# Kernel optimization log

Hardware: AMD Instinct MI355X
Metric: run time of the kernel (lower is better)

## Reference

```python
import jax, jax.numpy as jnp
import numpy as np

EPS = 1e-5


def setup_inputs() -> dict:
    key = jax.random.key(0)
    ks = jax.random.split(key, 8)
    b, n, l, e = 2, 16, 1024, 512
    qd, kd, vd = 64, 64, 64
    x = jax.random.normal(ks[0], (b, n, l, e), dtype=jnp.float32)
    past_kv = jax.random.normal(ks[1], (b, n, kd, vd), dtype=jnp.float32)
    s = 1.0 / np.sqrt(e)
    Wq = jax.random.normal(ks[2], (qd, e), dtype=jnp.float32) * s
    bq = jnp.zeros((qd,), dtype=jnp.float32)
    Wk = jax.random.normal(ks[3], (kd, e), dtype=jnp.float32) * s
    bk = jnp.zeros((kd,), dtype=jnp.float32)
    Wv = jax.random.normal(ks[4], (vd, e), dtype=jnp.float32) * s
    bv = jnp.zeros((vd,), dtype=jnp.float32)
    return {"x": x, "past_kv": past_kv, "Wq": Wq, "bq": bq,
            "Wk": Wk, "bk": bk, "Wv": Wv, "bv": bv}


def reference(x, past_kv, Wq, bq, Wk, bk, Wv, bv):
    b, n, l, e = x.shape
    # QKV projections on the last axis: [b,n,l,e] -> [b,n,l,d]
    q = jnp.einsum('bnle,de->bnld', x, Wq) + bq
    k = jnp.einsum('bnle,de->bnld', x, Wk) + bk
    v = jnp.einsum('bnle,de->bnld', x, Wv) + bv
    # RetNet per-head decay: 1 - 2^(-5-h), shape [1,n,1,1,1]
    decay = 1.0 - jnp.exp2(-5.0 - jnp.arange(n, dtype=jnp.float32))
    decay = decay.reshape(1, n, 1, 1, 1)
    # decayed state + per-position outer product k_t (x) v_t -> [b,n,l,kd,vd]
    current_kv = decay * past_kv[:, :, None, :, :] + k[..., :, None] * v[..., None, :]
    # Q-weighted reduction over k_dim -> [b,n,l,vd]
    out = jnp.einsum('bnlk,bnlkv->bnlv', q, current_kv)
    # F.group_norm(out, num_groups=n): per (b, head), normalize over (l, vd)
    mean = jnp.mean(out, axis=(2, 3), keepdims=True)
    var = jnp.var(out, axis=(2, 3), keepdims=True)
    out = (out - mean) * jax.lax.rsqrt(var + EPS)
    return out, current_kv
```

## Files before the change

### kernel.cpp

```cpp
#include <hip/hip_runtime.h>


constexpr int B  = 2;
constexpr int NH = 16;
constexpr int L  = 1024;
constexpr int E  = 512;
constexpr int D  = 64;
constexpr int M  = B * NH * L;
constexpr int NQKV = 192;
constexpr int BLK = 16;
constexpr int NBLKS = M / BLK;
constexpr float EPS = 1e-5f;

using short8 = __attribute__((ext_vector_type(8))) short;
using f32x4  = __attribute__((ext_vector_type(4))) float;

__device__ __forceinline__ unsigned short f2bf(float f) {
    union { float f; unsigned int u; } x; x.f = f;
    unsigned int u = x.u;
    return (unsigned short)((u + 0x7fffu + ((u >> 16) & 1u)) >> 16);
}

__global__ __launch_bounds__(256) void convw_kernel(
    const float* __restrict__ Wq, const float* __restrict__ Wk,
    const float* __restrict__ Wv, unsigned short* __restrict__ Wb)
{
    int idx = blockIdx.x * 256 + threadIdx.x;
    const float* src = (idx < 8192) ? Wq : (idx < 16384) ? Wk : Wv;
    int off = idx & 8191;
    float4 v = ((const float4*)src)[off];
    unsigned short o[4] = {f2bf(v.x), f2bf(v.y), f2bf(v.z), f2bf(v.w)};
    Wb[(size_t)idx * 4 + 0] = o[0];
    Wb[(size_t)idx * 4 + 1] = o[1];
    Wb[(size_t)idx * 4 + 2] = o[2];
    Wb[(size_t)idx * 4 + 3] = o[3];
}

__global__ __launch_bounds__(512) void proj_mfma_kernel(
    const float* __restrict__ x, const unsigned short* __restrict__ Wb,
    const float* __restrict__ bq, const float* __restrict__ bk,
    const float* __restrict__ bv,
    float* __restrict__ qkv)
{
    constexpr int BM = 128, BK = 64, LDP = 72;
    __shared__ unsigned short Xs[BM][LDP];
    __shared__ unsigned short Ws[NQKV][LDP];
    __shared__ float bias_s[NQKV];

    const int tid  = threadIdx.x;
    const int row0 = blockIdx.x * BM;
    if (tid < NQKV)
        bias_s[tid] = (tid < 64) ? bq[tid] : (tid < 128) ? bk[tid - 64] : bv[tid - 128];

    const int wid  = tid >> 6;
    const int lane = tid & 63;
    const int wr   = wid >> 2;
    const int wc   = wid & 3;
    const int l15  = lane & 15;
    const int lk   = (lane >> 4) * 8;

    const int xr = tid >> 2;
    const int xc = (tid & 3) * 16;

    f32x4 acc[4][3] = {};

    for (int k0 = 0; k0 < E; k0 += BK) {
        float4 xa[4];
        #pragma unroll
        for (int i = 0; i < 4; ++i)
            xa[i] = *(const float4*)&x[(size_t)(row0 + xr) * E + k0 + xc + i * 4];
        short8 wch[3];
        #pragma unroll
        for (int i = 0; i < 3; ++i) {
            int c = tid + i * 512;
            wch[i] = *(const short8*)&Wb[(size_t)(c >> 3) * E + k0 + (c & 7) * 8];
        }
        __syncthreads();
        unsigned short tmp[16];
        #pragma unroll
        for (int i = 0; i < 4; ++i) {
            tmp[i*4+0] = f2bf(xa[i].x); tmp[i*4+1] = f2bf(xa[i].y);
            tmp[i*4+2] = f2bf(xa[i].z); tmp[i*4+3] = f2bf(xa[i].w);
        }
        *(short8*)&Xs[xr][xc]     = *(short8*)&tmp[0];
        *(short8*)&Xs[xr][xc + 8] = *(short8*)&tmp[8];
        #pragma unroll
        for (int i = 0; i < 3; ++i) {
            int c = tid + i * 512;
            *(short8*)&Ws[c >> 3][(c & 7) * 8] = wch[i];
        }
        __syncthreads();

        #pragma unroll
        for (int kk = 0; kk < 2; ++kk) {
            short8 a[4], b[3];
            #pragma unroll
            for (int mi = 0; mi < 4; ++mi)
                a[mi] = *(const short8*)&Xs[wr * 64 + mi * 16 + l15][kk * 32 + lk];
            #pragma unroll
            for (int ni = 0; ni < 3; ++ni)
                b[ni] = *(const short8*)&Ws[wc * 48 + ni * 16 + l15][kk * 32 + lk];
            #pragma unroll
            for (int mi = 0; mi < 4; ++mi)
                #pragma unroll
                for (int ni = 0; ni < 3; ++ni)
                    acc[mi][ni] = __builtin_amdgcn_mfma_f32_16x16x32_bf16(
                        a[mi], b[ni], acc[mi][ni], 0, 0, 0);
        }
    }

    #pragma unroll
    for (int mi = 0; mi < 4; ++mi) {
        #pragma unroll
        for (int ni = 0; ni < 3; ++ni) {
            int col = wc * 48 + ni * 16 + l15;
            float bb = bias_s[col];
            #pragma unroll
            for (int j = 0; j < 4; ++j) {
                int row = wr * 64 + mi * 16 + (lane >> 4) * 4 + j;
                qkv[(size_t)(row0 + row) * NQKV + col] = acc[mi][ni][j] + bb;
            }
        }
    }
}

__global__ __launch_bounds__(256) void retention_kernel(
    const float* __restrict__ qkv,
    const float* __restrict__ past_kv,
    float* __restrict__ out_pre,
    float* __restrict__ ckv,
    float* __restrict__ partials)
{
    const int blk  = blockIdx.x;
    const int bn   = blk >> 6;
    const int pos0 = (blk & 63) * BLK;
    const int h    = bn & (NH - 1);
    const int tid  = threadIdx.x;
    const float decay = 1.0f - exp2f(-5.0f - (float)h);

    __shared__ float pkv_s[64 * 64];
    __shared__ float qkv_s[BLK * NQKV];
    __shared__ float qk_s[BLK];
    __shared__ float r1[256], r2[256];

    const float* pkv = past_kv + (size_t)bn * 4096;
    #pragma unroll
    for (int j = 0; j < 4; ++j) {
        int f = tid + j * 256;
        *(float4*)&pkv_s[f * 4] = *(const float4*)&pkv[f * 4];
    }
    const float* qrow = qkv + (size_t)(bn * L + pos0) * NQKV;
    #pragma unroll
    for (int j = 0; j < 3; ++j) {
        int f = tid + j * 256;
        *(float4*)&qkv_s[f * 4] = *(const float4*)&qrow[f * 4];
    }
    __syncthreads();

    {
        int pos = tid >> 4, c = tid & 15;
        const float* qp = &qkv_s[pos * NQKV];
        float p = 0.0f;
        #pragma unroll
        for (int j = 0; j < 4; ++j)
            p = fmaf(qp[c * 4 + j], qp[64 + c * 4 + j], p);
        p += __shfl_xor(p, 1); p += __shfl_xor(p, 2);
        p += __shfl_xor(p, 4); p += __shfl_xor(p, 8);
        if (c == 0) qk_s[pos] = p;
    }

    float4 p4[4];
    #pragma unroll
    for (int j = 0; j < 4; ++j)
        p4[j] = *(const float4*)&pkv_s[(tid + j * 256) * 4];
    __syncthreads();

    float* co = ckv + (size_t)(bn * L + pos0) * 4096;
    for (int pos = 0; pos < BLK; ++pos) {
        const float* ks = &qkv_s[pos * NQKV + 64];
        const float* vs = &qkv_s[pos * NQKV + 128];
        #pragma unroll
        for (int j = 0; j < 4; ++j) {
            int f = tid + j * 256;
            float kk = ks[f >> 4];
            float4 vv = *(const float4*)&vs[(f & 15) * 4];
            float4 r;
            r.x = fmaf(decay, p4[j].x, kk * vv.x);
            r.y = fmaf(decay, p4[j].y, kk * vv.y);
            r.z = fmaf(decay, p4[j].z, kk * vv.z);
            r.w = fmaf(decay, p4[j].w, kk * vv.w);
            *(float4*)&co[(size_t)pos * 4096 + f * 4] = r;
        }
    }

    const int wave = tid >> 6, vd = tid & 63;
    float accs[4] = {0.0f, 0.0f, 0.0f, 0.0f};
    for (int kd = 0; kd < 64; ++kd) {
        float pv = pkv_s[kd * 64 + vd];
        #pragma unroll
        for (int pp = 0; pp < 4; ++pp)
            accs[pp] = fmaf(qkv_s[(wave + pp * 4) * NQKV + kd], pv, accs[pp]);
    }
    float s1 = 0.0f, s2 = 0.0f;
    #pragma unroll
    for (int pp = 0; pp < 4; ++pp) {
        int pos = wave + pp * 4;
        float o = fmaf(decay, accs[pp],
                       qk_s[pos] * qkv_s[pos * NQKV + 128 + vd]);
        out_pre[(size_t)(bn * L + pos0 + pos) * D + vd] = o;
        s1 += o; s2 += o * o;
    }

    r1[tid] = s1; r2[tid] = s2;
    __syncthreads();
    for (int off = 128; off; off >>= 1) {
        if (tid < off) { r1[tid] += r1[tid + off]; r2[tid] += r2[tid + off]; }
        __syncthreads();
    }
    if (tid == 0) {
        partials[(size_t)blk * 2]     = r1[0];
        partials[(size_t)blk * 2 + 1] = r2[0];
    }
}

__global__ __launch_bounds__(64) void group_reduce_kernel(
    const float* __restrict__ partials, float* __restrict__ stats)
{
    const int g   = blockIdx.x;
    const int tid = threadIdx.x;
    float s1 = partials[(size_t)(g * 64 + tid) * 2];
    float s2 = partials[(size_t)(g * 64 + tid) * 2 + 1];
    #pragma unroll
    for (int off = 32; off; off >>= 1) {
        s1 += __shfl_down(s1, off);
        s2 += __shfl_down(s2, off);
    }
    if (tid == 0) {
        const float cnt = (float)(L * D);
        float mean = s1 / cnt;
        float var  = s2 / cnt - mean * mean;
        stats[g * 2]     = mean;
        stats[g * 2 + 1] = rsqrtf(var + EPS);
    }
}

__global__ __launch_bounds__(256) void normalize_kernel(
    float* __restrict__ out, const float* __restrict__ stats)
{
    int idx = blockIdx.x * 256 + threadIdx.x;
    int g = idx >> 14;
    float mean = stats[g * 2];
    float rstd = stats[g * 2 + 1];
    float4 v = ((const float4*)out)[idx];
    v.x = (v.x - mean) * rstd; v.y = (v.y - mean) * rstd;
    v.z = (v.z - mean) * rstd; v.w = (v.w - mean) * rstd;
    ((float4*)out)[idx] = v;
}

extern "C" void kernel_launch(void* const* d_in, const int* in_sizes, int n_in,
                              void* d_out, int out_size, void* d_ws, size_t ws_size,
                              hipStream_t stream)
{
    const float* x       = (const float*)d_in[0];
    const float* past_kv = (const float*)d_in[1];
    const float* Wq      = (const float*)d_in[2];
    const float* bq      = (const float*)d_in[3];
    const float* Wk      = (const float*)d_in[4];
    const float* bk      = (const float*)d_in[5];
    const float* Wv      = (const float*)d_in[6];
    const float* bv      = (const float*)d_in[7];

    float* out = (float*)d_out;
    float* ckv = out + (size_t)M * 64;

    unsigned short* Wb = (unsigned short*)(ckv + (size_t)M * 4096) - (size_t)NQKV * E;

    float* qkv      = (float*)d_ws;
    float* partials = qkv + (size_t)M * 192;
    float* stats    = partials + (size_t)NBLKS * 2;

    convw_kernel<<<96, 256, 0, stream>>>(Wq, Wk, Wv, Wb);
    proj_mfma_kernel<<<M / 128, 512, 0, stream>>>(x, Wb, bq, bk, bv, qkv);
    retention_kernel<<<NBLKS, 256, 0, stream>>>(qkv, past_kv, out, ckv, partials);
    group_reduce_kernel<<<32, 64, 0, stream>>>(partials, stats);
    normalize_kernel<<<(M * 16) / 256, 256, 0, stream>>>(out, stats);
}
```

Before: 146.8 us.

## Fuse QKV projection MFMA into retention kernel, drop qkv workspace round trip

```diff
diff --git a/kernel.cpp b/kernel.cpp
--- a/kernel.cpp
+++ b/kernel.cpp
@@ -29,108 +29,29 @@
     const float* src = (idx < 8192) ? Wq : (idx < 16384) ? Wk : Wv;
     int off = idx & 8191;
     float4 v = ((const float4*)src)[off];
-    unsigned short o[4] = {f2bf(v.x), f2bf(v.y), f2bf(v.z), f2bf(v.w)};
-    Wb[(size_t)idx * 4 + 0] = o[0];
-    Wb[(size_t)idx * 4 + 1] = o[1];
-    Wb[(size_t)idx * 4 + 2] = o[2];
-    Wb[(size_t)idx * 4 + 3] = o[3];
-}
-
-__global__ __launch_bounds__(512) void proj_mfma_kernel(
-    const float* __restrict__ x, const unsigned short* __restrict__ Wb,
+    Wb[(size_t)idx * 4 + 0] = f2bf(v.x);
+    Wb[(size_t)idx * 4 + 1] = f2bf(v.y);
+    Wb[(size_t)idx * 4 + 2] = f2bf(v.z);
+    Wb[(size_t)idx * 4 + 3] = f2bf(v.w);
+}
+
+__global__ __launch_bounds__(256) void fused_kernel(
+    const float* __restrict__ x,
+    const unsigned short* __restrict__ Wb,
     const float* __restrict__ bq, const float* __restrict__ bk,
     const float* __restrict__ bv,
-    float* __restrict__ qkv)
-{
-    constexpr int BM = 128, BK = 64, LDP = 72;
-    __shared__ unsigned short Xs[BM][LDP];
-    __shared__ unsigned short Ws[NQKV][LDP];
-    __shared__ float bias_s[NQKV];
-
-    const int tid  = threadIdx.x;
-    const int row0 = blockIdx.x * BM;
-    if (tid < NQKV)
-        bias_s[tid] = (tid < 64) ? bq[tid] : (tid < 128) ? bk[tid - 64] : bv[tid - 128];
-
-    const int wid  = tid >> 6;
-    const int lane = tid & 63;
-    const int wr   = wid >> 2;
-    const int wc   = wid & 3;
-    const int l15  = lane & 15;
-    const int lk   = (lane >> 4) * 8;
-
-    const int xr = tid >> 2;
-    const int xc = (tid & 3) * 16;
-
-    f32x4 acc[4][3] = {};
-
-    for (int k0 = 0; k0 < E; k0 += BK) {
-        float4 xa[4];
-        #pragma unroll
-        for (int i = 0; i < 4; ++i)
-            xa[i] = *(const float4*)&x[(size_t)(row0 + xr) * E + k0 + xc + i * 4];
-        short8 wch[3];
-        #pragma unroll
-        for (int i = 0; i < 3; ++i) {
-            int c = tid + i * 512;
-            wch[i] = *(const short8*)&Wb[(size_t)(c >> 3) * E + k0 + (c & 7) * 8];
-        }
-        __syncthreads();
-        unsigned short tmp[16];
-        #pragma unroll
-        for (int i = 0; i < 4; ++i) {
-            tmp[i*4+0] = f2bf(xa[i].x); tmp[i*4+1] = f2bf(xa[i].y);
-            tmp[i*4+2] = f2bf(xa[i].z); tmp[i*4+3] = f2bf(xa[i].w);
-        }
-        *(short8*)&Xs[xr][xc]     = *(short8*)&tmp[0];
-        *(short8*)&Xs[xr][xc + 8] = *(short8*)&tmp[8];
-        #pragma unroll
-        for (int i = 0; i < 3; ++i) {
-            int c = tid + i * 512;
-            *(short8*)&Ws[c >> 3][(c & 7) * 8] = wch[i];
-        }
-        __syncthreads();
-
-        #pragma unroll
-        for (int kk = 0; kk < 2; ++kk) {
-            short8 a[4], b[3];
-            #pragma unroll
-            for (int mi = 0; mi < 4; ++mi)
-                a[mi] = *(const short8*)&Xs[wr * 64 + mi * 16 + l15][kk * 32 + lk];
-            #pragma unroll
-            for (int ni = 0; ni < 3; ++ni)
-                b[ni] = *(const short8*)&Ws[wc * 48 + ni * 16 + l15][kk * 32 + lk];
-            #pragma unroll
-            for (int mi = 0; mi < 4; ++mi)
-                #pragma unroll
-                for (int ni = 0; ni < 3; ++ni)
-                    acc[mi][ni] = __builtin_amdgcn_mfma_f32_16x16x32_bf16(
-                        a[mi], b[ni], acc[mi][ni], 0, 0, 0);
-        }
-    }
-
-    #pragma unroll
-    for (int mi = 0; mi < 4; ++mi) {
-        #pragma unroll
-        for (int ni = 0; ni < 3; ++ni) {
-            int col = wc * 48 + ni * 16 + l15;
-            float bb = bias_s[col];
-            #pragma unroll
-            for (int j = 0; j < 4; ++j) {
-                int row = wr * 64 + mi * 16 + (lane >> 4) * 4 + j;
-                qkv[(size_t)(row0 + row) * NQKV + col] = acc[mi][ni][j] + bb;
-            }
-        }
-    }
-}
-
-__global__ __launch_bounds__(256) void retention_kernel(
-    const float* __restrict__ qkv,
     const float* __restrict__ past_kv,
     float* __restrict__ out_pre,
     float* __restrict__ ckv,
     float* __restrict__ partials)
 {
+    constexpr int LDP = 520;
+    __shared__ unsigned short Xs[BLK][LDP];
+    __shared__ float qkv_s[BLK * NQKV];
+    __shared__ float bias_s[NQKV];
+    __shared__ float qk_s[BLK];
+    __shared__ float r1[256], r2[256];
+
     const int blk  = blockIdx.x;
     const int bn   = blk >> 6;
     const int pos0 = (blk & 63) * BLK;
@@ -138,22 +59,53 @@
     const int tid  = threadIdx.x;
     const float decay = 1.0f - exp2f(-5.0f - (float)h);
 
-    __shared__ float pkv_s[64 * 64];
-    __shared__ float qkv_s[BLK * NQKV];
-    __shared__ float qk_s[BLK];
-    __shared__ float r1[256], r2[256];
+    if (tid < NQKV)
+        bias_s[tid] = (tid < 64) ? bq[tid] : (tid < 128) ? bk[tid - 64] : bv[tid - 128];
+
+    const float* xrow = x + (size_t)(bn * L + pos0) * E;
+    #pragma unroll
+    for (int j = 0; j < 8; ++j) {
+        int f   = tid + j * 256;
+        int row = f >> 7;
+        int c4  = f & 127;
+        float4 xv = *(const float4*)&xrow[f * 4];
+        unsigned short hlf[4] = {f2bf(xv.x), f2bf(xv.y), f2bf(xv.z), f2bf(xv.w)};
+        *(uint2*)&Xs[row][c4 * 4] = *(uint2*)hlf;
+    }
 
     const float* pkv = past_kv + (size_t)bn * 4096;
-    #pragma unroll
-    for (int j = 0; j < 4; ++j) {
-        int f = tid + j * 256;
-        *(float4*)&pkv_s[f * 4] = *(const float4*)&pkv[f * 4];
-    }
-    const float* qrow = qkv + (size_t)(bn * L + pos0) * NQKV;
-    #pragma unroll
-    for (int j = 0; j < 3; ++j) {
-        int f = tid + j * 256;
-        *(float4*)&qkv_s[f * 4] = *(const float4*)&qrow[f * 4];
+    float4 p4[4];
+    #pragma unroll
+    for (int j = 0; j < 4; ++j)
+        p4[j] = *(const float4*)&pkv[(tid + j * 256) * 4];
+
+    __syncthreads();
+
+    const int wid  = tid >> 6;
+    const int lane = tid & 63;
+    const int l15  = lane & 15;
+    const int lkE  = (lane >> 4) * 8;
+
+    f32x4 acc[3] = {};
+    #pragma unroll 4
+    for (int kt = 0; kt < 16; ++kt) {
+        short8 a = *(const short8*)&Xs[l15][kt * 32 + lkE];
+        #pragma unroll
+        for (int ni = 0; ni < 3; ++ni) {
+            int col = wid * 48 + ni * 16 + l15;
+            short8 b = *(const short8*)&Wb[(size_t)col * E + kt * 32 + lkE];
+            acc[ni] = __builtin_amdgcn_mfma_f32_16x16x32_bf16(a, b, acc[ni], 0, 0, 0);
+        }
+    }
+    #pragma unroll
+    for (int ni = 0; ni < 3; ++ni) {
+        int col = wid * 48 + ni * 16 + l15;
+        float bb = bias_s[col];
+        #pragma unroll
+        for (int j = 0; j < 4; ++j) {
+            int pos = (lane >> 4) * 4 + j;
+            qkv_s[pos * NQKV + col] = acc[ni][j] + bb;
+        }
     }
     __syncthreads();
 
@@ -168,11 +120,6 @@
         p += __shfl_xor(p, 4); p += __shfl_xor(p, 8);
         if (c == 0) qk_s[pos] = p;
     }
-
-    float4 p4[4];
-    #pragma unroll
-    for (int j = 0; j < 4; ++j)
-        p4[j] = *(const float4*)&pkv_s[(tid + j * 256) * 4];
     __syncthreads();
 
     float* co = ckv + (size_t)(bn * L + pos0) * 4096;
@@ -195,8 +142,9 @@
 
     const int wave = tid >> 6, vd = tid & 63;
     float accs[4] = {0.0f, 0.0f, 0.0f, 0.0f};
+    #pragma unroll 8
     for (int kd = 0; kd < 64; ++kd) {
-        float pv = pkv_s[kd * 64 + vd];
+        float pv = pkv[kd * 64 + vd];
         #pragma unroll
         for (int pp = 0; pp < 4; ++pp)
             accs[pp] = fmaf(qkv_s[(wave + pp * 4) * NQKV + kd], pv, accs[pp]);
@@ -273,15 +221,13 @@
     float* out = (float*)d_out;
     float* ckv = out + (size_t)M * 64;
 
-    unsigned short* Wb = (unsigned short*)(ckv + (size_t)M * 4096) - (size_t)NQKV * E;
-
-    float* qkv      = (float*)d_ws;
-    float* partials = qkv + (size_t)M * 192;
+    unsigned short* Wb = (unsigned short*)d_ws;
+    float* partials = (float*)(Wb + (size_t)NQKV * E);
     float* stats    = partials + (size_t)NBLKS * 2;
 
     convw_kernel<<<96, 256, 0, stream>>>(Wq, Wk, Wv, Wb);
-    proj_mfma_kernel<<<M / 128, 512, 0, stream>>>(x, Wb, bq, bk, bv, qkv);
-    retention_kernel<<<NBLKS, 256, 0, stream>>>(qkv, past_kv, out, ckv, partials);
+    fused_kernel<<<NBLKS, 256, 0, stream>>>(x, Wb, bq, bk, bv, past_kv,
+                                            out, ckv, partials);
     group_reduce_kernel<<<32, 64, 0, stream>>>(partials, stats);
     normalize_kernel<<<(M * 16) / 256, 256, 0, stream>>>(out, stats);
 }
```

Result: slower. 159.6 us (+8.7%).

## Store QKV intermediate in bf16 and enlarge retention blocks to 32 positions

Applied to the files above, without the earlier changes.

```diff
diff --git a/kernel.cpp b/kernel.cpp
--- a/kernel.cpp
+++ b/kernel.cpp
@@ -8,7 +8,7 @@
 constexpr int D  = 64;
 constexpr int M  = B * NH * L;
 constexpr int NQKV = 192;
-constexpr int BLK = 16;
+constexpr int BLK = 32;
 constexpr int NBLKS = M / BLK;
 constexpr float EPS = 1e-5f;
 
@@ -20,6 +20,10 @@
     unsigned int u = x.u;
     return (unsigned short)((u + 0x7fffu + ((u >> 16) & 1u)) >> 16);
 }
+__device__ __forceinline__ float bf2f(unsigned short h) {
+    union { unsigned int u; float f; } x; x.u = ((unsigned int)h) << 16;
+    return x.f;
+}
 
 __global__ __launch_bounds__(256) void convw_kernel(
     const float* __restrict__ Wq, const float* __restrict__ Wk,
@@ -29,18 +33,17 @@
     const float* src = (idx < 8192) ? Wq : (idx < 16384) ? Wk : Wv;
     int off = idx & 8191;
     float4 v = ((const float4*)src)[off];
-    unsigned short o[4] = {f2bf(v.x), f2bf(v.y), f2bf(v.z), f2bf(v.w)};
-    Wb[(size_t)idx * 4 + 0] = o[0];
-    Wb[(size_t)idx * 4 + 1] = o[1];
-    Wb[(size_t)idx * 4 + 2] = o[2];
-    Wb[(size_t)idx * 4 + 3] = o[3];
+    Wb[(size_t)idx * 4 + 0] = f2bf(v.x);
+    Wb[(size_t)idx * 4 + 1] = f2bf(v.y);
+    Wb[(size_t)idx * 4 + 2] = f2bf(v.z);
+    Wb[(size_t)idx * 4 + 3] = f2bf(v.w);
 }
 
 __global__ __launch_bounds__(512) void proj_mfma_kernel(
     const float* __restrict__ x, const unsigned short* __restrict__ Wb,
     const float* __restrict__ bq, const float* __restrict__ bk,
     const float* __restrict__ bv,
-    float* __restrict__ qkv)
+    unsigned short* __restrict__ qkvb)
 {
     constexpr int BM = 128, BK = 64, LDP = 72;
     __shared__ unsigned short Xs[BM][LDP];
@@ -118,108 +121,106 @@
             #pragma unroll
             for (int j = 0; j < 4; ++j) {
                 int row = wr * 64 + mi * 16 + (lane >> 4) * 4 + j;
-                qkv[(size_t)(row0 + row) * NQKV + col] = acc[mi][ni][j] + bb;
+                qkvb[(size_t)(row0 + row) * NQKV + col] = f2bf(acc[mi][ni][j] + bb);
             }
         }
     }
 }
 
-__global__ __launch_bounds__(256) void retention_kernel(
-    const float* __restrict__ qkv,
+__global__ __launch_bounds__(512) void retention_kernel(
+    const unsigned short* __restrict__ qkvb,
     const float* __restrict__ past_kv,
     float* __restrict__ out_pre,
     float* __restrict__ ckv,
     float* __restrict__ partials)
 {
     const int blk  = blockIdx.x;
-    const int bn   = blk >> 6;
-    const int pos0 = (blk & 63) * BLK;
+    const int bn   = blk >> 5;
+    const int pos0 = (blk & 31) * BLK;
     const int h    = bn & (NH - 1);
     const int tid  = threadIdx.x;
     const float decay = 1.0f - exp2f(-5.0f - (float)h);
 
     __shared__ float pkv_s[64 * 64];
-    __shared__ float qkv_s[BLK * NQKV];
+    __shared__ unsigned short qkv_s[BLK * NQKV];
     __shared__ float qk_s[BLK];
-    __shared__ float r1[256], r2[256];
+    __shared__ float red[16];
 
     const float* pkv = past_kv + (size_t)bn * 4096;
-    #pragma unroll
-    for (int j = 0; j < 4; ++j) {
-        int f = tid + j * 256;
-        *(float4*)&pkv_s[f * 4] = *(const float4*)&pkv[f * 4];
-    }
-    const float* qrow = qkv + (size_t)(bn * L + pos0) * NQKV;
-    #pragma unroll
-    for (int j = 0; j < 3; ++j) {
-        int f = tid + j * 256;
-        *(float4*)&qkv_s[f * 4] = *(const float4*)&qrow[f * 4];
-    }
+    float4 p4[2];
+    #pragma unroll
+    for (int j = 0; j < 2; ++j) {
+        p4[j] = *(const float4*)&pkv[(tid + j * 512) * 4];
+        *(float4*)&pkv_s[(tid + j * 512) * 4] = p4[j];
+    }
+    const unsigned short* qrow = qkvb + (size_t)(bn * L + pos0) * NQKV;
+    for (int f = tid; f < 768; f += 512)
+        ((uint4*)qkv_s)[f] = ((const uint4*)qrow)[f];
     __syncthreads();
 
     {
         int pos = tid >> 4, c = tid & 15;
-        const float* qp = &qkv_s[pos * NQKV];
+        const unsigned short* qp = &qkv_s[pos * NQKV];
         float p = 0.0f;
         #pragma unroll
         for (int j = 0; j < 4; ++j)
-            p = fmaf(qp[c * 4 + j], qp[64 + c * 4 + j], p);
+            p = fmaf(bf2f(qp[c * 4 + j]), bf2f(qp[64 + c * 4 + j]), p);
         p += __shfl_xor(p, 1); p += __shfl_xor(p, 2);
         p += __shfl_xor(p, 4); p += __shfl_xor(p, 8);
         if (c == 0) qk_s[pos] = p;
     }
 
-    float4 p4[4];
-    #pragma unroll
-    for (int j = 0; j < 4; ++j)
-        p4[j] = *(const float4*)&pkv_s[(tid + j * 256) * 4];
-    __syncthreads();
-
     float* co = ckv + (size_t)(bn * L + pos0) * 4096;
     for (int pos = 0; pos < BLK; ++pos) {
-        const float* ks = &qkv_s[pos * NQKV + 64];
-        const float* vs = &qkv_s[pos * NQKV + 128];
-        #pragma unroll
-        for (int j = 0; j < 4; ++j) {
-            int f = tid + j * 256;
-            float kk = ks[f >> 4];
-            float4 vv = *(const float4*)&vs[(f & 15) * 4];
+        const unsigned short* ks = &qkv_s[pos * NQKV + 64];
+        const unsigned short* vs = &qkv_s[pos * NQKV + 128];
+        #pragma unroll
+        for (int j = 0; j < 2; ++j) {
+            int f = tid + j * 512;
+            float kk = bf2f(ks[f >> 4]);
+            const unsigned short* vp = &vs[(f & 15) * 4];
             float4 r;
-            r.x = fmaf(decay, p4[j].x, kk * vv.x);
-            r.y = fmaf(decay, p4[j].y, kk * vv.y);
-            r.z = fmaf(decay, p4[j].z, kk * vv.z);
-            r.w = fmaf(decay, p4[j].w, kk * vv.w);
+            r.x = fmaf(decay, p4[j].x, kk * bf2f(vp[0]));
+            r.y = fmaf(decay, p4[j].y, kk * bf2f(vp[1]));
+            r.z = fmaf(decay, p4[j].z, kk * bf2f(vp[2]));
+            r.w = fmaf(decay, p4[j].w, kk * bf2f(vp[3]));
             *(float4*)&co[(size_t)pos * 4096 + f * 4] = r;
         }
     }
-
-    const int wave = tid >> 6, vd = tid & 63;
+    __syncthreads();
+
+    const int wave = tid >> 6, lane = tid & 63;
+    const int vd = lane;
     float accs[4] = {0.0f, 0.0f, 0.0f, 0.0f};
     for (int kd = 0; kd < 64; ++kd) {
         float pv = pkv_s[kd * 64 + vd];
         #pragma unroll
         for (int pp = 0; pp < 4; ++pp)
-            accs[pp] = fmaf(qkv_s[(wave + pp * 4) * NQKV + kd], pv, accs[pp]);
+            accs[pp] = fmaf(bf2f(qkv_s[(wave + pp * 8) * NQKV + kd]), pv, accs[pp]);
     }
     float s1 = 0.0f, s2 = 0.0f;
     #pragma unroll
     for (int pp = 0; pp < 4; ++pp) {
-        int pos = wave + pp * 4;
+        int pos = wave + pp * 8;
         float o = fmaf(decay, accs[pp],
-                       qk_s[pos] * qkv_s[pos * NQKV + 128 + vd]);
+                       qk_s[pos] * bf2f(qkv_s[pos * NQKV + 128 + vd]));
         out_pre[(size_t)(bn * L + pos0 + pos) * D + vd] = o;
         s1 += o; s2 += o * o;
     }
 
-    r1[tid] = s1; r2[tid] = s2;
+    #pragma unroll
+    for (int off = 32; off; off >>= 1) {
+        s1 += __shfl_down(s1, off);
+        s2 += __shfl_down(s2, off);
+    }
+    if (lane == 0) { red[wave * 2] = s1; red[wave * 2 + 1] = s2; }
     __syncthreads();
-    for (int off = 128; off; off >>= 1) {
-        if (tid < off) { r1[tid] += r1[tid + off]; r2[tid] += r2[tid + off]; }
-        __syncthreads();
-    }
     if (tid == 0) {
-        partials[(size_t)blk * 2]     = r1[0];
-        partials[(size_t)blk * 2 + 1] = r2[0];
+        float a = 0.0f, b2 = 0.0f;
+        #pragma unroll
+        for (int w = 0; w < 8; ++w) { a += red[w * 2]; b2 += red[w * 2 + 1]; }
+        partials[(size_t)blk * 2]     = a;
+        partials[(size_t)blk * 2 + 1] = b2;
     }
 }
 
@@ -228,10 +229,13 @@
 {
     const int g   = blockIdx.x;
     const int tid = threadIdx.x;
-    float s1 = partials[(size_t)(g * 64 + tid) * 2];
-    float s2 = partials[(size_t)(g * 64 + tid) * 2 + 1];
-    #pragma unroll
-    for (int off = 32; off; off >>= 1) {
+    float s1 = 0.0f, s2 = 0.0f;
+    if (tid < 32) {
+        s1 = partials[(size_t)(g * 32 + tid) * 2];
+        s2 = partials[(size_t)(g * 32 + tid) * 2 + 1];
+    }
+    #pragma unroll
+    for (int off = 16; off; off >>= 1) {
         s1 += __shfl_down(s1, off);
         s2 += __shfl_down(s2, off);
     }
@@ -273,15 +277,14 @@
     float* out = (float*)d_out;
     float* ckv = out + (size_t)M * 64;
 
-    unsigned short* Wb = (unsigned short*)(ckv + (size_t)M * 4096) - (size_t)NQKV * E;
-
-    float* qkv      = (float*)d_ws;
-    float* partials = qkv + (size_t)M * 192;
+    unsigned short* Wb   = (unsigned short*)d_ws;
+    unsigned short* qkvb = Wb + (size_t)NQKV * E;
+    float* partials = (float*)(qkvb + (size_t)M * NQKV);
     float* stats    = partials + (size_t)NBLKS * 2;
 
     convw_kernel<<<96, 256, 0, stream>>>(Wq, Wk, Wv, Wb);
-    proj_mfma_kernel<<<M / 128, 512, 0, stream>>>(x, Wb, bq, bk, bv, qkv);
-    retention_kernel<<<NBLKS, 256, 0, stream>>>(qkv, past_kv, out, ckv, partials);
+    proj_mfma_kernel<<<M / 128, 512, 0, stream>>>(x, Wb, bq, bk, bv, qkvb);
+    retention_kernel<<<NBLKS, 512, 0, stream>>>(qkvb, past_kv, out, ckv, partials);
     group_reduce_kernel<<<32, 64, 0, stream>>>(partials, stats);
     normalize_kernel<<<(M * 16) / 256, 256, 0, stream>>>(out, stats);
 }
```

After: 139.7 us. 1.05x faster.
